# Performance work log

Measured on AMD Instinct MI355X. Metric: run time of the kernel, lower is better.

## Reference

```python
import jax, jax.numpy as jnp
import numpy as np

N_NODES = 100000
F_IN = 128


def gcn_conv(x, W, b, src, dst, num_nodes):
    """PyG GCNConv: add self-loops, symmetric deg^-1/2 normalization,
    aggregate then linear (equivalently linear then aggregate)."""
    h = x @ W  # [N, F_out]
    # self-loops
    loop = jnp.arange(num_nodes, dtype=src.dtype)
    s = jnp.concatenate([src, loop])
    d = jnp.concatenate([dst, loop])
    ones = jnp.ones(s.shape[0], dtype=x.dtype)
    deg = jax.ops.segment_sum(ones, d, num_segments=num_nodes)  # in-degree w/ self-loops
    dinv = jnp.where(deg > 0, jax.lax.rsqrt(deg), 0.0)
    norm = dinv[s] * dinv[d]  # [E+N]
    msg = h[s] * norm[:, None]  # gather + scale
    out = jax.ops.segment_sum(msg, d, num_segments=num_nodes)  # scatter-add
    return out + b


def setup_inputs() -> dict:
    key = jax.random.key(0)
    k1, k2, k3, k4 = jax.random.split(key, 4)
    x = jax.random.normal(k1, (N_NODES, F_IN), dtype=jnp.float32)
    edge_index = jax.random.randint(k2, (2, 600000), 0, N_NODES, dtype=jnp.int64)
    # GCNConv weights (glorot-ish scale) and zero biases
    W1 = jax.random.normal(k3, (F_IN, F_IN), dtype=jnp.float32) / np.sqrt(F_IN)
    b1 = jnp.zeros((F_IN,), dtype=jnp.float32)
    W2 = jax.random.normal(k4, (F_IN, 2 * F_IN), dtype=jnp.float32) / np.sqrt(F_IN)
    b2 = jnp.zeros((2 * F_IN,), dtype=jnp.float32)
    return {"x": x, "edge_index": edge_index, "W1": W1, "b1": b1, "W2": W2, "b2": b2}


def reference(x, edge_index, W1, b1, W2, b2):
    src, dst = edge_index[0], edge_index[1]
    n = x.shape[0]
    h = gcn_conv(x, W1, b1, src, dst, n)
    h = jax.nn.relu(h)  # dropout is identity in eval mode
    h = gcn_conv(h, W2, b2, src, dst, n)
    h = jax.nn.relu(h)
    return jnp.mean(h, axis=0)  # [2*F_IN]
```

## Files before the change

kernel.cpp:

```cpp
#include <hip/hip_runtime.h>


typedef __attribute__((ext_vector_type(8))) short short8;
typedef __attribute__((ext_vector_type(4))) float f32x4;

__device__ __forceinline__ float b2f(unsigned short u) {
    union { unsigned int i; float f; } c;
    c.i = ((unsigned int)u) << 16;
    return c.f;
}
__device__ __forceinline__ unsigned short f2b(float x) {
    union { float f; unsigned int i; } c;
    c.f = x;
    unsigned int r = c.i + 0x7FFFu + ((c.i >> 16) & 1u);
    return (unsigned short)(r >> 16);
}

__global__ void k_detect(const int* __restrict__ ei, int E, int* __restrict__ flag) {
    __shared__ int anyv[4];
    int t = threadIdx.x;
    int v = 0;
#pragma unroll
    for (int r = 0; r < 4; ++r) {
        long long k = (long long)(t * 4 + r) * E >> 10;
        v |= ei[2 * (int)k + 1];
    }
    unsigned long long m = __ballot(v != 0);
    if ((t & 63) == 0) anyv[t >> 6] = (m != 0ull) ? 1 : 0;
    __syncthreads();
    if (t == 0) flag[0] = anyv[0] | anyv[1] | anyv[2] | anyv[3];
}

__device__ __forceinline__ int edge_idx(const void* ei, int is64, int which,
                                        int E, int e) {
    if (is64) return (int)((const long long*)ei)[(size_t)which * E + e];
    return ((const int*)ei)[(size_t)which * E + e];
}

__global__ void k_zero_int(int* p, int n) {
    int i = blockIdx.x * 256 + threadIdx.x;
    if (i < n) p[i] = 0;
}

__global__ void k_count(const void* __restrict__ ei, const int* __restrict__ flag,
                        int* __restrict__ counts, int E) {
    int e = blockIdx.x * 256 + threadIdx.x;
    if (e >= E) return;
    int is64 = (*flag == 0);
    int d = edge_idx(ei, is64, 1, E, e);
    atomicAdd(&counts[d], 1);
}

__global__ void k_dinv(const int* __restrict__ counts, float* __restrict__ dinv,
                       int n) {
    int i = blockIdx.x * 256 + threadIdx.x;
    if (i < n) dinv[i] = rsqrtf(1.0f + (float)counts[i]);
}

__global__ void k_scan1(const int* __restrict__ counts, int* __restrict__ offs,
                        int* __restrict__ blockSums, int n) {
    __shared__ int tmp[256];
    int t = threadIdx.x;
    int i = blockIdx.x * 256 + t;
    int my = (i < n) ? counts[i] : 0;
    tmp[t] = my;
    __syncthreads();
    for (int off = 1; off < 256; off <<= 1) {
        int v = (t >= off) ? tmp[t - off] : 0;
        __syncthreads();
        tmp[t] += v;
        __syncthreads();
    }
    if (i < n) offs[i] = tmp[t] - my;
    if (t == 255) blockSums[blockIdx.x] = tmp[255];
}

__global__ void k_scan2(int* __restrict__ blockSums, int nb) {
    __shared__ int tmp[512];
    __shared__ int carry;
    int t = threadIdx.x;
    if (t == 0) carry = 0;
    __syncthreads();
    for (int base = 0; base < nb; base += 512) {
        int i = base + t;
        int my = (i < nb) ? blockSums[i] : 0;
        tmp[t] = my;
        __syncthreads();
        for (int off = 1; off < 512; off <<= 1) {
            int v = (t >= off) ? tmp[t - off] : 0;
            __syncthreads();
            tmp[t] += v;
            __syncthreads();
        }
        if (i < nb) blockSums[i] = carry + tmp[t] - my;
        __syncthreads();
        if (t == 0) carry += tmp[511];
        __syncthreads();
    }
}

__global__ void k_scan3(int* __restrict__ offs, const int* __restrict__ blockSums,
                        int* __restrict__ cursor, int n) {
    int i = blockIdx.x * 256 + threadIdx.x;
    if (i < n) {
        int o = offs[i] + blockSums[blockIdx.x];
        offs[i] = o;
        cursor[i] = o;
    }
}

__global__ void k_fill_csr(const void* __restrict__ ei, const int* __restrict__ flag,
                           int* __restrict__ cursor, int* __restrict__ csr, int E) {
    int e = blockIdx.x * 256 + threadIdx.x;
    if (e >= E) return;
    int is64 = (*flag == 0);
    int s = edge_idx(ei, is64, 0, E, e);
    int d = edge_idx(ei, is64, 1, E, e);
    int pos = atomicAdd(&cursor[d], 1);
    csr[pos] = s;
}

__global__ void k_cvt_x(const float* __restrict__ x, unsigned short* __restrict__ xb,
                        int n4) {
    int i = blockIdx.x * 256 + threadIdx.x;
    if (i >= n4) return;
    float4 v = reinterpret_cast<const float4*>(x)[i];
    ushort4 o;
    o.x = f2b(v.x); o.y = f2b(v.y); o.z = f2b(v.z); o.w = f2b(v.w);
    reinterpret_cast<ushort4*>(xb)[i] = o;
}

__global__ void k_cvt_wt(const float* __restrict__ W, unsigned short* __restrict__ WT,
                         int KOUT, int total) {
    int idx = blockIdx.x * 256 + threadIdx.x;
    if (idx >= total) return;
    int k = idx / KOUT, n = idx % KOUT;
    WT[(size_t)n * 128 + k] = f2b(W[idx]);
}

__global__ __launch_bounds__(256) void k_gather_b(const unsigned short* __restrict__ h,
                                                  const float* __restrict__ dinv,
                                                  const int* __restrict__ offs,
                                                  const int* __restrict__ counts,
                                                  const int* __restrict__ csr,
                                                  unsigned short* __restrict__ g,
                                                  int N) {
    int node = blockIdx.x * 16 + (threadIdx.x >> 4);
    int l16 = threadIdx.x & 15;
    if (node >= N) return;
    const short8* h8 = reinterpret_cast<const short8*>(h);
    float dd = dinv[node];
    float w0 = dd * dd;
    size_t rowu = (size_t)node * 16 + l16;
    short8 sv = h8[rowu];
    float a[8];
#pragma unroll
    for (int j = 0; j < 8; ++j) a[j] = b2f((unsigned short)sv[j]) * w0;
    int beg = offs[node], cnt = counts[node];
    for (int e = 0; e < cnt; ++e) {
        int s = csr[beg + e];
        float w = dinv[s] * dd;
        short8 v = h8[(size_t)s * 16 + l16];
#pragma unroll
        for (int j = 0; j < 8; ++j) a[j] = fmaf(b2f((unsigned short)v[j]), w, a[j]);
    }
    short8 o;
#pragma unroll
    for (int j = 0; j < 8; ++j) o[j] = (short)f2b(a[j]);
    reinterpret_cast<short8*>(g)[rowu] = o;
}

template <int KOUT, bool REDUCE, int CHUNK>
__global__ __launch_bounds__(256) void k_mgemm(const unsigned short* __restrict__ A,
                                               const unsigned short* __restrict__ WT,
                                               const float* __restrict__ bias,
                                               unsigned short* __restrict__ C,
                                               float* __restrict__ partials, int N) {
    constexpr int NFW = KOUT / 64;
    const int tid = threadIdx.x;
    const int wave = tid >> 6, lane = tid & 63;
    const int l15 = lane & 15, lg = lane >> 4;
    const int colbase = wave * (KOUT / 4);

    short8 breg[NFW][4];
    float bv[NFW];
#pragma unroll
    for (int nf = 0; nf < NFW; ++nf) {
        int col = colbase + nf * 16 + l15;
        bv[nf] = bias[col];
#pragma unroll
        for (int kk = 0; kk < 4; ++kk)
            breg[nf][kk] = *reinterpret_cast<const short8*>(
                WT + (size_t)col * 128 + kk * 32 + lg * 8);
    }

    float psum[NFW];
#pragma unroll
    for (int nf = 0; nf < NFW; ++nf) psum[nf] = 0.f;

    const int NT = (N + 15) / 16;
    const int t0 = blockIdx.x * CHUNK;
    const int tend = (t0 + CHUNK < NT) ? t0 + CHUNK : NT;

#pragma unroll 2
    for (int t = t0; t < tend; ++t) {
        const int rows = t * 16;
        const int arow = rows + l15;
        short8 a[4];
        const bool rv = arow < N;
#pragma unroll
        for (int kk = 0; kk < 4; ++kk)
            a[kk] = rv ? *reinterpret_cast<const short8*>(
                             A + (size_t)arow * 128 + kk * 32 + lg * 8)
                       : (short8){0, 0, 0, 0, 0, 0, 0, 0};

        f32x4 acc[NFW];
#pragma unroll
        for (int nf = 0; nf < NFW; ++nf) acc[nf] = (f32x4){0.f, 0.f, 0.f, 0.f};
#pragma unroll
        for (int kk = 0; kk < 4; ++kk)
#pragma unroll
            for (int nf = 0; nf < NFW; ++nf)
                acc[nf] = __builtin_amdgcn_mfma_f32_16x16x32_bf16(
                    a[kk], breg[nf][kk], acc[nf], 0, 0, 0);

        if (!REDUCE) {
#pragma unroll
            for (int nf = 0; nf < NFW; ++nf) {
                int col = colbase + nf * 16 + l15;
#pragma unroll
                for (int r = 0; r < 4; ++r) {
                    int rr = rows + lg * 4 + r;
                    if (rr < N)
                        C[(size_t)rr * KOUT + col] =
                            f2b(fmaxf(acc[nf][r] + bv[nf], 0.f));
                }
            }
        } else {
#pragma unroll
            for (int nf = 0; nf < NFW; ++nf) {
#pragma unroll
                for (int r = 0; r < 4; ++r) {
                    int rr = rows + lg * 4 + r;
                    if (rr < N) psum[nf] += fmaxf(acc[nf][r] + bv[nf], 0.f);
                }
            }
        }
    }

    if (REDUCE) {
#pragma unroll
        for (int nf = 0; nf < NFW; ++nf) {
            float s = psum[nf];
            s += __shfl_xor(s, 16);
            s += __shfl_xor(s, 32);
            if (lg == 0)
                partials[(size_t)blockIdx.x * KOUT + colbase + nf * 16 + l15] = s;
        }
    }
}

__global__ void k_reduce1(const float* __restrict__ partials, float* __restrict__ p2,
                          int NB) {
    int c = threadIdx.x;
    float sum = 0.f;
    for (int r = blockIdx.x; r < NB; r += 16)
        sum += partials[(size_t)r * 256 + c];
    p2[blockIdx.x * 256 + c] = sum;
}

__global__ void k_reduce2(const float* __restrict__ p2, float* __restrict__ out,
                          float invN) {
    int c = threadIdx.x;
    float sum = 0.f;
#pragma unroll
    for (int b = 0; b < 16; ++b) sum += p2[b * 256 + c];
    out[c] = sum * invN;
}

extern "C" void kernel_launch(void* const* d_in, const int* in_sizes, int n_in,
                              void* d_out, int out_size, void* d_ws, size_t ws_size,
                              hipStream_t stream) {
    const float* x  = (const float*)d_in[0];
    const void*  ei = d_in[1];
    const float* W1 = (const float*)d_in[2];
    const float* b1 = (const float*)d_in[3];
    const float* W2 = (const float*)d_in[4];
    const float* b2 = (const float*)d_in[5];
    float* out = (float*)d_out;

    const int N = in_sizes[0] / 128;
    const int E = in_sizes[1] / 2;
    const int nb = (N + 255) / 256;
    constexpr int CHUNK = 8;
    const int NT = (N + 15) / 16;
    const int NBLK = (NT + CHUNK - 1) / CHUNK;

    char* ws = (char*)d_ws;
    size_t off = 0;
    auto alloc = [&](size_t bytes) {
        char* p = ws + off;
        off += (bytes + 255) & ~(size_t)255;
        return p;
    };
    int*            flag      = (int*)alloc(4);
    int*            counts    = (int*)alloc((size_t)N * 4);
    int*            offs      = (int*)alloc((size_t)N * 4);
    int*            cursor    = (int*)alloc((size_t)N * 4);
    int*            blockSums = (int*)alloc((size_t)nb * 4);
    float*          dinv      = (float*)alloc((size_t)N * 4);
    int*            csr       = (int*)alloc((size_t)E * 4);
    float*          partials  = (float*)alloc((size_t)NBLK * 256 * 4);
    float*          p2        = (float*)alloc((size_t)16 * 256 * 4);
    unsigned short* wt1       = (unsigned short*)alloc((size_t)128 * 128 * 2);
    unsigned short* wt2       = (unsigned short*)alloc((size_t)256 * 128 * 2);
    unsigned short* xb        = (unsigned short*)alloc((size_t)N * 128 * 2);
    unsigned short* g1        = (unsigned short*)alloc((size_t)N * 128 * 2);
    unsigned short* a1r       = (unsigned short*)alloc((size_t)N * 128 * 2);
    unsigned short* g2        = xb;

    k_detect<<<1, 256, 0, stream>>>((const int*)ei, E, flag);
    k_zero_int<<<nb, 256, 0, stream>>>(counts, N);
    k_count<<<(E + 255) / 256, 256, 0, stream>>>(ei, flag, counts, E);
    k_dinv<<<nb, 256, 0, stream>>>(counts, dinv, N);
    k_scan1<<<nb, 256, 0, stream>>>(counts, offs, blockSums, N);
    k_scan2<<<1, 512, 0, stream>>>(blockSums, nb);
    k_scan3<<<nb, 256, 0, stream>>>(offs, blockSums, cursor, N);
    k_fill_csr<<<(E + 255) / 256, 256, 0, stream>>>(ei, flag, cursor, csr, E);

    k_cvt_x<<<(N * 32 + 255) / 256, 256, 0, stream>>>(x, xb, N * 32);
    k_cvt_wt<<<(128 * 128 + 255) / 256, 256, 0, stream>>>(W1, wt1, 128, 128 * 128);
    k_cvt_wt<<<(128 * 256 + 255) / 256, 256, 0, stream>>>(W2, wt2, 256, 128 * 256);

    k_gather_b<<<(N + 15) / 16, 256, 0, stream>>>(xb, dinv, offs, counts, csr, g1, N);
    k_mgemm<128, false, CHUNK><<<NBLK, 256, 0, stream>>>(g1, wt1, b1, a1r, nullptr, N);

    k_gather_b<<<(N + 15) / 16, 256, 0, stream>>>(a1r, dinv, offs, counts, csr, g2, N);
    k_mgemm<256, true, CHUNK><<<NBLK, 256, 0, stream>>>(g2, wt2, b2, nullptr, partials, N);
    k_reduce1<<<16, 256, 0, stream>>>(partials, p2, NBLK);
    k_reduce2<<<1, 256, 0, stream>>>(p2, out, 1.0f / (float)N);
}
```

Measured before the change: 240.6 us.

## Precompute edge weights into CSR, fuse dinv into scan, software-pipeline gather

Each CSR entry now holds the source index together with its precomputed normalization weight. This removes the dependent dinv[s] lookup from the gather inner loop. The dinv computation moves into the scan kernel and the zeroing kernel becomes a memset, which removes two launches. The gather kernel processes several nodes per thread group and prefetches the next neighbor row before doing the FMAs, at the cost of doubling the CSR size that must be read.

Result: faster. 219.5 us (-8.8%).

```diff
diff --git a/kernel.cpp b/kernel.cpp
--- a/kernel.cpp
+++ b/kernel.cpp
@@ -35,11 +35,6 @@
                                         int E, int e) {
     if (is64) return (int)((const long long*)ei)[(size_t)which * E + e];
     return ((const int*)ei)[(size_t)which * E + e];
-}
-
-__global__ void k_zero_int(int* p, int n) {
-    int i = blockIdx.x * 256 + threadIdx.x;
-    if (i < n) p[i] = 0;
 }
 
 __global__ void k_count(const void* __restrict__ ei, const int* __restrict__ flag,
@@ -51,18 +46,14 @@
     atomicAdd(&counts[d], 1);
 }
 
-__global__ void k_dinv(const int* __restrict__ counts, float* __restrict__ dinv,
-                       int n) {
-    int i = blockIdx.x * 256 + threadIdx.x;
-    if (i < n) dinv[i] = rsqrtf(1.0f + (float)counts[i]);
-}
-
 __global__ void k_scan1(const int* __restrict__ counts, int* __restrict__ offs,
-                        int* __restrict__ blockSums, int n) {
+                        int* __restrict__ blockSums, float* __restrict__ dinv,
+                        int n) {
     __shared__ int tmp[256];
     int t = threadIdx.x;
     int i = blockIdx.x * 256 + t;
     int my = (i < n) ? counts[i] : 0;
+    if (i < n) dinv[i] = rsqrtf(1.0f + (float)my);
     tmp[t] = my;
     __syncthreads();
     for (int off = 1; off < 256; off <<= 1) {
@@ -110,14 +101,15 @@
 }
 
 __global__ void k_fill_csr(const void* __restrict__ ei, const int* __restrict__ flag,
-                           int* __restrict__ cursor, int* __restrict__ csr, int E) {
+                           const float* __restrict__ dinv, int* __restrict__ cursor,
+                           int2* __restrict__ csr2, int E) {
     int e = blockIdx.x * 256 + threadIdx.x;
     if (e >= E) return;
     int is64 = (*flag == 0);
     int s = edge_idx(ei, is64, 0, E, e);
     int d = edge_idx(ei, is64, 1, E, e);
     int pos = atomicAdd(&cursor[d], 1);
-    csr[pos] = s;
+    csr2[pos] = make_int2(s, __float_as_int(dinv[s] * dinv[d]));
 }
 
 __global__ void k_cvt_x(const float* __restrict__ x, unsigned short* __restrict__ xb,
@@ -138,36 +130,52 @@
     WT[(size_t)n * 128 + k] = f2b(W[idx]);
 }
 
+template <int CHUNK>
 __global__ __launch_bounds__(256) void k_gather_b(const unsigned short* __restrict__ h,
                                                   const float* __restrict__ dinv,
                                                   const int* __restrict__ offs,
                                                   const int* __restrict__ counts,
-                                                  const int* __restrict__ csr,
+                                                  const int2* __restrict__ csr2,
                                                   unsigned short* __restrict__ g,
                                                   int N) {
-    int node = blockIdx.x * 16 + (threadIdx.x >> 4);
-    int l16 = threadIdx.x & 15;
-    if (node >= N) return;
+    const int grp = threadIdx.x >> 4, l16 = threadIdx.x & 15;
     const short8* h8 = reinterpret_cast<const short8*>(h);
-    float dd = dinv[node];
-    float w0 = dd * dd;
-    size_t rowu = (size_t)node * 16 + l16;
-    short8 sv = h8[rowu];
-    float a[8];
-#pragma unroll
-    for (int j = 0; j < 8; ++j) a[j] = b2f((unsigned short)sv[j]) * w0;
-    int beg = offs[node], cnt = counts[node];
-    for (int e = 0; e < cnt; ++e) {
-        int s = csr[beg + e];
-        float w = dinv[s] * dd;
-        short8 v = h8[(size_t)s * 16 + l16];
-#pragma unroll
-        for (int j = 0; j < 8; ++j) a[j] = fmaf(b2f((unsigned short)v[j]), w, a[j]);
-    }
-    short8 o;
-#pragma unroll
-    for (int j = 0; j < 8; ++j) o[j] = (short)f2b(a[j]);
-    reinterpret_cast<short8*>(g)[rowu] = o;
+    const int base = blockIdx.x * (CHUNK * 16) + grp;
+
+    for (int i = 0; i < CHUNK; ++i) {
+        const int node = base + i * 16;
+        if (node >= N) break;
+        const float dd = dinv[node];
+        const float w0 = dd * dd;
+        const size_t rowu = (size_t)node * 16 + l16;
+        short8 sv = h8[rowu];
+        float a[8];
+#pragma unroll
+        for (int j = 0; j < 8; ++j) a[j] = b2f((unsigned short)sv[j]) * w0;
+
+        const int beg = offs[node], cnt = counts[node];
+        if (cnt > 0) {
+            int2 p = csr2[beg];
+            short8 v = h8[(size_t)p.x * 16 + l16];
+            for (int e = 1; e < cnt; ++e) {
+                int2 pn = csr2[beg + e];
+                short8 vn = h8[(size_t)pn.x * 16 + l16];
+                float w = __int_as_float(p.y);
+#pragma unroll
+                for (int j = 0; j < 8; ++j)
+                    a[j] = fmaf(b2f((unsigned short)v[j]), w, a[j]);
+                p = pn; v = vn;
+            }
+            float w = __int_as_float(p.y);
+#pragma unroll
+            for (int j = 0; j < 8; ++j)
+                a[j] = fmaf(b2f((unsigned short)v[j]), w, a[j]);
+        }
+        short8 o;
+#pragma unroll
+        for (int j = 0; j < 8; ++j) o[j] = (short)f2b(a[j]);
+        reinterpret_cast<short8*>(g)[rowu] = o;
+    }
 }
 
 template <int KOUT, bool REDUCE, int CHUNK>
@@ -292,9 +300,11 @@
     const int N = in_sizes[0] / 128;
     const int E = in_sizes[1] / 2;
     const int nb = (N + 255) / 256;
-    constexpr int CHUNK = 8;
+    constexpr int GCHUNK = 4;
+    constexpr int MCHUNK = 8;
     const int NT = (N + 15) / 16;
-    const int NBLK = (NT + CHUNK - 1) / CHUNK;
+    const int NBLK = (NT + MCHUNK - 1) / MCHUNK;
+    const int GBLK = (N + GCHUNK * 16 - 1) / (GCHUNK * 16);
 
     char* ws = (char*)d_ws;
     size_t off = 0;
@@ -309,7 +319,7 @@
     int*            cursor    = (int*)alloc((size_t)N * 4);
     int*            blockSums = (int*)alloc((size_t)nb * 4);
     float*          dinv      = (float*)alloc((size_t)N * 4);
-    int*            csr       = (int*)alloc((size_t)E * 4);
+    int2*           csr2      = (int2*)alloc((size_t)E * 8);
     float*          partials  = (float*)alloc((size_t)NBLK * 256 * 4);
     float*          p2        = (float*)alloc((size_t)16 * 256 * 4);
     unsigned short* wt1       = (unsigned short*)alloc((size_t)128 * 128 * 2);
@@ -320,23 +330,22 @@
     unsigned short* g2        = xb;
 
     k_detect<<<1, 256, 0, stream>>>((const int*)ei, E, flag);
-    k_zero_int<<<nb, 256, 0, stream>>>(counts, N);
+    hipMemsetAsync(counts, 0, (size_t)N * 4, stream);
     k_count<<<(E + 255) / 256, 256, 0, stream>>>(ei, flag, counts, E);
-    k_dinv<<<nb, 256, 0, stream>>>(counts, dinv, N);
-    k_scan1<<<nb, 256, 0, stream>>>(counts, offs, blockSums, N);
+    k_scan1<<<nb, 256, 0, stream>>>(counts, offs, blockSums, dinv, N);
     k_scan2<<<1, 512, 0, stream>>>(blockSums, nb);
     k_scan3<<<nb, 256, 0, stream>>>(offs, blockSums, cursor, N);
-    k_fill_csr<<<(E + 255) / 256, 256, 0, stream>>>(ei, flag, cursor, csr, E);
+    k_fill_csr<<<(E + 255) / 256, 256, 0, stream>>>(ei, flag, dinv, cursor, csr2, E);
 
     k_cvt_x<<<(N * 32 + 255) / 256, 256, 0, stream>>>(x, xb, N * 32);
     k_cvt_wt<<<(128 * 128 + 255) / 256, 256, 0, stream>>>(W1, wt1, 128, 128 * 128);
     k_cvt_wt<<<(128 * 256 + 255) / 256, 256, 0, stream>>>(W2, wt2, 256, 128 * 256);
 
-    k_gather_b<<<(N + 15) / 16, 256, 0, stream>>>(xb, dinv, offs, counts, csr, g1, N);
-    k_mgemm<128, false, CHUNK><<<NBLK, 256, 0, stream>>>(g1, wt1, b1, a1r, nullptr, N);
-
-    k_gather_b<<<(N + 15) / 16, 256, 0, stream>>>(a1r, dinv, offs, counts, csr, g2, N);
-    k_mgemm<256, true, CHUNK><<<NBLK, 256, 0, stream>>>(g2, wt2, b2, nullptr, partials, N);
+    k_gather_b<GCHUNK><<<GBLK, 256, 0, stream>>>(xb, dinv, offs, counts, csr2, g1, N);
+    k_mgemm<128, false, MCHUNK><<<NBLK, 256, 0, stream>>>(g1, wt1, b1, a1r, nullptr, N);
+
+    k_gather_b<GCHUNK><<<GBLK, 256, 0, stream>>>(a1r, dinv, offs, counts, csr2, g2, N);
+    k_mgemm<256, true, MCHUNK><<<NBLK, 256, 0, stream>>>(g2, wt2, b2, nullptr, partials, N);
     k_reduce1<<<16, 256, 0, stream>>>(partials, p2, NBLK);
     k_reduce2<<<1, 256, 0, stream>>>(p2, out, 1.0f / (float)N);
 }
```
